# Performance work log

Hardware: AMD Instinct MI355X
Metric: run time of the kernel (lower is better)

## Reference

```python
import jax, jax.numpy as jnp
import numpy as np

B, D, H = 64, 768, 512            # batch, bert hidden, classifier hidden_dim
G0, C0 = 8192, 8                  # level-0 meta labels, children per meta
G1, C1 = 65536, 11                # level-1 meta labels, children per meta (incl. pad)
L = 670091                        # num labels; pad id == L, table has L+1 rows
K1, K2 = 32, 64                   # candidates_topk


def setup_inputs() -> dict:
    key = jax.random.key(0)
    ks = jax.random.split(key, 14)
    rn = lambda k, shp, s=1.0: jax.random.normal(k, shp, jnp.float32) * s
    w = 0.02  # xavier-ish init scale
    inp = {
        'feat5':   rn(ks[0], (B, D)),
        'feat8':   rn(ks[1], (B, D)),
        'featcat': rn(ks[2], (B, 3 * D)),
        'W0': rn(ks[3], (D, H), w),     'b0': jnp.zeros((H,), jnp.float32),
        'W1': rn(ks[4], (D, H), w),     'b1': jnp.zeros((H,), jnp.float32),
        'W2': rn(ks[5], (3 * D, H), w), 'b2': jnp.zeros((H,), jnp.float32),
        'E0': rn(ks[6], (G0, H), w),
        'E1': rn(ks[7], (G1, H), w),
        # padding row (index L) is zero, per self.Cn[-1].weight[-1].data.fill_(0)
        'E2': rn(ks[8], (L + 1, H), w).at[-1].set(0.0),
        'g0': jax.random.randint(ks[9], (G0, C0), 0, G1, dtype=jnp.int32),
        'g1': jax.random.randint(ks[10], (G1, C1), 0, L + 1, dtype=jnp.int32),
    }
    return inp


def reference(feat5, feat8, featcat, W0, b0, W1, b1, W2, b2, E0, E1, E2, g0, g1):
    gelu = lambda x: jax.nn.gelu(x, approximate=False)  # torch nn.GELU default (erf)
    # Cn_hidden (dropout is identity at eval)
    h0 = gelu(feat5 @ W0 + b0)      # [B,H]
    h1 = gelu(feat8 @ W1 + b1)      # [B,H]
    h2 = gelu(featcat @ W2 + b2)    # [B,H]

    # ---- level 0: score all G0 meta-labels (dense bmm) ----
    logits0 = jnp.einsum('gh,bh->bg', E0, h0)            # [B,G0]
    p0 = jax.nn.sigmoid(logits0)
    prev0 = jax.lax.stop_gradient(p0)                    # prev_logits = scores.detach()

    # ---- level 1: topk routing + gather + bmm ----
    sc1, idx1 = jax.lax.top_k(prev0, K1)                 # [B,K1]; prev_cands is arange -> identity map
    cands1 = g0[idx1].reshape(B, K1 * C0)                # [B,K1*C0] level-1 meta ids
    gsc1 = jnp.repeat(sc1, C0, axis=1)                   # candidates_scores flattened
    logits1 = jnp.einsum('bch,bh->bc', E1[cands1], h1)   # [B,K1*C0]
    p1 = jax.nn.sigmoid(logits1)
    w1 = p1 * gsc1
    prev1 = jax.lax.stop_gradient(p1)

    # ---- level 2 (final): topk routing into padded label groups ----
    sc2, idx2 = jax.lax.top_k(prev1, K2)                 # [B,K2]
    meta2 = jnp.take_along_axis(cands1, idx2, axis=1)    # indices into g1
    cands2 = g1[meta2].reshape(B, K2 * C1)               # [B,K2*C1] label ids (L == pad)
    gsc2 = jnp.repeat(sc2, C1, axis=1)
    logits2 = jnp.einsum('bch,bh->bc', E2[cands2], h2)   # pad rows of E2 are 0 -> logit 0
    # torch: where(logits==0, -inf, logits).sigmoid() -> pad positions score 0
    p2 = jnp.where(logits2 == 0.0, jnp.float32(0.0), jax.nn.sigmoid(logits2))
    w2 = p2 * gsc2

    return (p0, p1, p2, w1, w2, cands1, cands2)
```

## Files before the change

kernel.cpp:

```cpp
#include <hip/hip_runtime.h>
#include <math.h>

#define BB 64
#define D0 768
#define D2 2304
#define HH 512
#define BBHH (BB*HH)
#define NG0 8192
#define NC0 8
#define NCH1 11
#define TK1 32
#define TK2 64
#define NC1 (TK1*NC0)
#define NC2 (TK2*NCH1)
#define SP0 6
#define SP1 6
#define SP2 18

__device__ __forceinline__ float sigmoidf_(float x){ return 1.0f/(1.0f+expf(-x)); }
__device__ __forceinline__ float geluf_(float x){ return 0.5f*x*(1.0f+erff(x*0.70710678118654752f)); }
__device__ __forceinline__ unsigned long long maxu64_(unsigned long long a, unsigned long long b){ return a>b?a:b; }

__device__ __forceinline__ unsigned long long bitonic256_desc(
    unsigned long long key, int tid, unsigned long long* sbuf)
{
  #pragma unroll
  for (int k = 2; k <= 256; k <<= 1) {
    #pragma unroll
    for (int j = k >> 1; j > 0; j >>= 1) {
      unsigned long long other;
      if (j >= 64) {
        __syncthreads();
        sbuf[tid] = key;
        __syncthreads();
        other = sbuf[tid ^ j];
      } else {
        other = __shfl_xor(key, j, 64);
      }
      bool keep_max = ((tid & j) == 0) == ((tid & k) == 0);
      key = keep_max ? (key > other ? key : other)
                     : (key < other ? key : other);
    }
  }
  return key;
}

__global__ __launch_bounds__(256) void gemm_h_kernel(
    const float* __restrict__ feat5, const float* __restrict__ feat8,
    const float* __restrict__ featcat,
    const float* __restrict__ W0, const float* __restrict__ W1,
    const float* __restrict__ W2, float* __restrict__ P)
{
  int bid = blockIdx.x;
  const float* X; const float* W; int Dm, split, tile; float* Pb;
  if (bid < 48)      { X=feat5;   W=W0; Dm=D0; split=bid%6;  tile=bid/6;
                       Pb=P + (size_t)split*BBHH; }
  else if (bid < 96) { int l=bid-48; X=feat8; W=W1; Dm=D0; split=l%6; tile=l/6;
                       Pb=P + (size_t)(SP0+split)*BBHH; }
  else               { int l=bid-96; X=featcat; W=W2; Dm=D2; split=l%18; tile=l/18;
                       Pb=P + (size_t)(SP0+SP1+split)*BBHH; }
  int k0 = split*128;
  int jt = tile*64;
  __shared__ __align__(16) float At[32][68];
  __shared__ __align__(16) float Bt[32][68];
  int tid = threadIdx.x;
  int ti = tid >> 4, tj = tid & 15;
  float acc[4][4] = {};
  for (int ks = 0; ks < 128; ks += 32) {
    #pragma unroll
    for (int it = 0; it < 2; ++it) {
      int q = tid + it*256;
      int b = q & 63, kq = q >> 6;
      float4 v = *(const float4*)(X + (size_t)b*Dm + k0 + ks + kq*4);
      At[kq*4+0][b]=v.x; At[kq*4+1][b]=v.y; At[kq*4+2][b]=v.z; At[kq*4+3][b]=v.w;
    }
    #pragma unroll
    for (int it = 0; it < 2; ++it) {
      int q = tid + it*256;
      int j4 = q & 15, kk = q >> 4;
      float4 v = *(const float4*)(W + (size_t)(k0+ks+kk)*HH + jt + j4*4);
      *(float4*)&Bt[kk][j4*4] = v;
    }
    __syncthreads();
    #pragma unroll
    for (int k = 0; k < 32; ++k) {
      float4 a = *(const float4*)&At[k][ti*4];
      float4 b = *(const float4*)&Bt[k][tj*4];
      float av[4] = {a.x,a.y,a.z,a.w};
      float bv[4] = {b.x,b.y,b.z,b.w};
      #pragma unroll
      for (int r=0;r<4;++r)
        #pragma unroll
        for (int c=0;c<4;++c) acc[r][c] += av[r]*bv[c];
    }
    __syncthreads();
  }
  #pragma unroll
  for (int r=0;r<4;++r)
    #pragma unroll
    for (int c=0;c<4;++c) {
      int b = ti*4+r; int j = jt + tj*4 + c;
      Pb[(size_t)b*HH + j] = acc[r][c];
    }
}

__global__ __launch_bounds__(256) void level0_kernel(
    const float* __restrict__ P, const float* __restrict__ b0v,
    const float* __restrict__ E0, float* __restrict__ p0out)
{
  int bid = blockIdx.x;
  int btile = bid & 1;
  int gt = bid >> 1;
  __shared__ __align__(16) float At[32][36];
  __shared__ __align__(16) float Bt[32][68];
  int tid = threadIdx.x;
  int ti = tid >> 4, tj = tid & 15;
  float acc[2][4] = {};
  for (int ks = 0; ks < HH; ks += 32) {
    {
      int bb = tid & 31, kq = tid >> 5;
      float4 a = make_float4(0.f,0.f,0.f,0.f);
      #pragma unroll
      for (int s=0;s<SP0;++s){
        const float4 p = *(const float4*)(P + (size_t)s*BBHH
                           + (size_t)(btile*32+bb)*HH + ks + kq*4);
        a.x+=p.x; a.y+=p.y; a.z+=p.z; a.w+=p.w;
      }
      float4 bv = *(const float4*)(b0v + ks + kq*4);
      At[kq*4+0][bb]=geluf_(a.x+bv.x);
      At[kq*4+1][bb]=geluf_(a.y+bv.y);
      At[kq*4+2][bb]=geluf_(a.z+bv.z);
      At[kq*4+3][bb]=geluf_(a.w+bv.w);
    }
    #pragma unroll
    for (int it=0; it<2; ++it) {
      int q = tid + it*256; int g = q & 63, kq = q >> 6;
      float4 v = *(const float4*)(E0 + (size_t)(gt*64+g)*HH + ks + kq*4);
      Bt[kq*4+0][g]=v.x; Bt[kq*4+1][g]=v.y; Bt[kq*4+2][g]=v.z; Bt[kq*4+3][g]=v.w;
    }
    __syncthreads();
    #pragma unroll
    for (int k=0;k<32;++k) {
      float2 a = *(const float2*)&At[k][ti*2];
      float4 b = *(const float4*)&Bt[k][tj*4];
      float av[2] = {a.x,a.y};
      float bv[4] = {b.x,b.y,b.z,b.w};
      #pragma unroll
      for (int r=0;r<2;++r)
        #pragma unroll
        for (int c=0;c<4;++c) acc[r][c] += av[r]*bv[c];
    }
    __syncthreads();
  }
  #pragma unroll
  for (int r=0;r<2;++r)
    #pragma unroll
    for (int c=0;c<4;++c) {
      int b = btile*32 + ti*2 + r;
      int g = gt*64 + tj*4 + c;
      p0out[(size_t)b*NG0 + g] = sigmoidf_(acc[r][c]);
    }
}

__global__ __launch_bounds__(256) void topk1_kernel(
    const float* __restrict__ p0, const int* __restrict__ g0,
    const float* __restrict__ P, const float* __restrict__ b1v,
    float* __restrict__ h1out,
    int* __restrict__ cands1_i, float* __restrict__ gsc1, float* __restrict__ out_c1)
{
  int b = blockIdx.x, tid = threadIdx.x;
  {
    int j = tid*2;
    float ax=0.f, ay=0.f;
    #pragma unroll
    for (int s=0;s<SP1;++s){
      float2 v = *(const float2*)(P + (size_t)(SP0+s)*BBHH + (size_t)b*HH + j);
      ax += v.x; ay += v.y;
    }
    float2 bv = *(const float2*)(b1v + j);
    h1out[(size_t)b*HH + j]   = geluf_(ax + bv.x);
    h1out[(size_t)b*HH + j+1] = geluf_(ay + bv.y);
  }
  const float* row = p0 + (size_t)b*NG0;
  const float4* rp = (const float4*)(row + tid*32);
  unsigned long long m = 0ull;
  #pragma unroll
  for (int t=0;t<8;++t){
    float4 v = rp[t];
    unsigned i0 = (unsigned)(tid*32 + t*4);
    m = maxu64_(m, ((unsigned long long)__float_as_uint(v.x)<<32) | (unsigned long long)(0xFFFFFFFFu-(i0+0)));
    m = maxu64_(m, ((unsigned long long)__float_as_uint(v.y)<<32) | (unsigned long long)(0xFFFFFFFFu-(i0+1)));
    m = maxu64_(m, ((unsigned long long)__float_as_uint(v.z)<<32) | (unsigned long long)(0xFFFFFFFFu-(i0+2)));
    m = maxu64_(m, ((unsigned long long)__float_as_uint(v.w)<<32) | (unsigned long long)(0xFFFFFFFFu-(i0+3)));
  }
  __shared__ unsigned long long sbuf[256];
  __shared__ unsigned long long slist[256];
  __shared__ int scnt;
  __shared__ float s_sc[TK1];
  __shared__ int   s_idx[TK1];
  if (tid==0) scnt = 0;
  __syncthreads();
  unsigned long long sk = bitonic256_desc(m, tid, sbuf);
  __syncthreads();
  sbuf[tid] = sk;
  __syncthreads();
  unsigned long long t32 = sbuf[31];
  __syncthreads();
  #pragma unroll
  for (int t=0;t<8;++t){
    float4 v = rp[t];
    unsigned i0 = (unsigned)(tid*32 + t*4);
    unsigned long long k0 = ((unsigned long long)__float_as_uint(v.x)<<32) | (unsigned long long)(0xFFFFFFFFu-(i0+0));
    unsigned long long k1 = ((unsigned long long)__float_as_uint(v.y)<<32) | (unsigned long long)(0xFFFFFFFFu-(i0+1));
    unsigned long long k2 = ((unsigned long long)__float_as_uint(v.z)<<32) | (unsigned long long)(0xFFFFFFFFu-(i0+2));
    unsigned long long k3 = ((unsigned long long)__float_as_uint(v.w)<<32) | (unsigned long long)(0xFFFFFFFFu-(i0+3));
    if (k0 >= t32) { int p = atomicAdd(&scnt,1); if (p<256) slist[p]=k0; }
    if (k1 >= t32) { int p = atomicAdd(&scnt,1); if (p<256) slist[p]=k1; }
    if (k2 >= t32) { int p = atomicAdd(&scnt,1); if (p<256) slist[p]=k2; }
    if (k3 >= t32) { int p = atomicAdd(&scnt,1); if (p<256) slist[p]=k3; }
  }
  __syncthreads();
  int cnt = scnt;
  unsigned long long key2 = (tid < cnt) ? slist[tid] : 0ull;
  key2 = bitonic256_desc(key2, tid, sbuf);
  __syncthreads();
  sbuf[tid] = key2;
  __syncthreads();
  if (tid < TK1) {
    unsigned long long w = sbuf[tid];
    s_idx[tid] = (int)(0xFFFFFFFFu - (unsigned)(w & 0xFFFFFFFFull));
    s_sc[tid]  = __uint_as_float((unsigned)(w>>32));
  }
  __syncthreads();
  if (tid < NC1) {
    int k = tid >> 3, c = tid & 7;
    int cand = g0[(size_t)s_idx[k]*NC0 + c];
    cands1_i[(size_t)b*NC1+tid] = cand;
    gsc1[(size_t)b*NC1+tid] = s_sc[k];
    out_c1[(size_t)b*NC1+tid] = (float)cand;
  }
}

__global__ __launch_bounds__(256) void level1_kernel(
    const float* __restrict__ h1, const int* __restrict__ cands1_i,
    const float* __restrict__ gsc1, const float* __restrict__ E1,
    float* __restrict__ p1out, float* __restrict__ w1out)
{
  int b = blockIdx.x; int tid = threadIdx.x;
  int lane = tid & 63, wid = tid >> 6;
  const float4* h4 = (const float4*)(h1 + (size_t)b*HH);
  float4 ha = h4[lane*2], hb = h4[lane*2+1];
  int cbase = blockIdx.y*16 + wid*4;
  const int* ci = cands1_i + (size_t)b*NC1 + cbase;
  int id0=ci[0], id1=ci[1], id2=ci[2], id3=ci[3];
  const float4* e0 = (const float4*)(E1 + (size_t)id0*HH);
  const float4* e1 = (const float4*)(E1 + (size_t)id1*HH);
  const float4* e2 = (const float4*)(E1 + (size_t)id2*HH);
  const float4* e3 = (const float4*)(E1 + (size_t)id3*HH);
  float4 a0=e0[lane*2], c0=e0[lane*2+1];
  float4 a1=e1[lane*2], c1=e1[lane*2+1];
  float4 a2=e2[lane*2], c2=e2[lane*2+1];
  float4 a3=e3[lane*2], c3=e3[lane*2+1];
  float s0 = ha.x*a0.x+ha.y*a0.y+ha.z*a0.z+ha.w*a0.w + hb.x*c0.x+hb.y*c0.y+hb.z*c0.z+hb.w*c0.w;
  float s1 = ha.x*a1.x+ha.y*a1.y+ha.z*a1.z+ha.w*a1.w + hb.x*c1.x+hb.y*c1.y+hb.z*c1.z+hb.w*c1.w;
  float s2 = ha.x*a2.x+ha.y*a2.y+ha.z*a2.z+ha.w*a2.w + hb.x*c2.x+hb.y*c2.y+hb.z*c2.z+hb.w*c2.w;
  float s3 = ha.x*a3.x+ha.y*a3.y+ha.z*a3.z+ha.w*a3.w + hb.x*c3.x+hb.y*c3.y+hb.z*c3.z+hb.w*c3.w;
  #pragma unroll
  for (int off=1; off<64; off<<=1) {
    s0 += __shfl_xor(s0, off);
    s1 += __shfl_xor(s1, off);
    s2 += __shfl_xor(s2, off);
    s3 += __shfl_xor(s3, off);
  }
  if (lane==0) {
    const float* gs = gsc1 + (size_t)b*NC1 + cbase;
    float p;
    p = sigmoidf_(s0); p1out[(size_t)b*NC1+cbase+0]=p; w1out[(size_t)b*NC1+cbase+0]=p*gs[0];
    p = sigmoidf_(s1); p1out[(size_t)b*NC1+cbase+1]=p; w1out[(size_t)b*NC1+cbase+1]=p*gs[1];
    p = sigmoidf_(s2); p1out[(size_t)b*NC1+cbase+2]=p; w1out[(size_t)b*NC1+cbase+2]=p*gs[2];
    p = sigmoidf_(s3); p1out[(size_t)b*NC1+cbase+3]=p; w1out[(size_t)b*NC1+cbase+3]=p*gs[3];
  }
}

__global__ __launch_bounds__(256) void topk2_kernel(
    const float* __restrict__ p1, const int* __restrict__ cands1_i,
    const int* __restrict__ g1,
    const float* __restrict__ P, const float* __restrict__ b2v,
    float* __restrict__ h2out,
    int* __restrict__ cands2_i, float* __restrict__ gsc2, float* __restrict__ out_c2)
{
  int b = blockIdx.x, tid = threadIdx.x;
  {
    int j = tid*2;
    float ax=0.f, ay=0.f;
    #pragma unroll
    for (int s=0;s<SP2;++s){
      float2 v = *(const float2*)(P + (size_t)(SP0+SP1+s)*BBHH + (size_t)b*HH + j);
      ax += v.x; ay += v.y;
    }
    float2 bv = *(const float2*)(b2v + j);
    h2out[(size_t)b*HH + j]   = geluf_(ax + bv.x);
    h2out[(size_t)b*HH + j+1] = geluf_(ay + bv.y);
  }
  float v = p1[(size_t)b*NC1 + tid];
  unsigned long long key = ((unsigned long long)__float_as_uint(v)<<32) |
                           (unsigned long long)(0xFFFFFFFFu - (unsigned)tid);
  __shared__ unsigned long long sbuf[256];
  __shared__ float s_sc[TK2];
  __shared__ int   s_idx[TK2];
  key = bitonic256_desc(key, tid, sbuf);
  __syncthreads();
  sbuf[tid] = key;
  __syncthreads();
  if (tid < TK2) {
    unsigned long long w = sbuf[tid];
    s_idx[tid] = (int)(0xFFFFFFFFu - (unsigned)(w & 0xFFFFFFFFull));
    s_sc[tid]  = __uint_as_float((unsigned)(w>>32));
  }
  __syncthreads();
  for (int e=tid; e<NC2; e+=256) {
    int k = e/NCH1, c = e - k*NCH1;
    int meta = cands1_i[(size_t)b*NC1 + s_idx[k]];
    int cand = g1[(size_t)meta*NCH1 + c];
    cands2_i[(size_t)b*NC2+e] = cand;
    gsc2[(size_t)b*NC2+e] = s_sc[k];
    out_c2[(size_t)b*NC2+e] = (float)cand;
  }
}

__global__ __launch_bounds__(256) void level2_kernel(
    const float* __restrict__ h2, const int* __restrict__ cands2_i,
    const float* __restrict__ gsc2, const float* __restrict__ E2,
    float* __restrict__ p2out, float* __restrict__ w2out)
{
  int b = blockIdx.x; int tid = threadIdx.x;
  int lane = tid & 63, wid = tid >> 6;
  const float4* h4 = (const float4*)(h2 + (size_t)b*HH);
  float4 ha = h4[lane*2], hb = h4[lane*2+1];
  int cbase = blockIdx.y*16 + wid*4;
  const int* ci = cands2_i + (size_t)b*NC2 + cbase;
  int id0=ci[0], id1=ci[1], id2=ci[2], id3=ci[3];
  const float4* e0 = (const float4*)(E2 + (size_t)id0*HH);
  const float4* e1 = (const float4*)(E2 + (size_t)id1*HH);
  const float4* e2 = (const float4*)(E2 + (size_t)id2*HH);
  const float4* e3 = (const float4*)(E2 + (size_t)id3*HH);
  float4 a0=e0[lane*2], c0=e0[lane*2+1];
  float4 a1=e1[lane*2], c1=e1[lane*2+1];
  float4 a2=e2[lane*2], c2=e2[lane*2+1];
  float4 a3=e3[lane*2], c3=e3[lane*2+1];
  float s0 = ha.x*a0.x+ha.y*a0.y+ha.z*a0.z+ha.w*a0.w + hb.x*c0.x+hb.y*c0.y+hb.z*c0.z+hb.w*c0.w;
  float s1 = ha.x*a1.x+ha.y*a1.y+ha.z*a1.z+ha.w*a1.w + hb.x*c1.x+hb.y*c1.y+hb.z*c1.z+hb.w*c1.w;
  float s2 = ha.x*a2.x+ha.y*a2.y+ha.z*a2.z+ha.w*a2.w + hb.x*c2.x+hb.y*c2.y+hb.z*c2.z+hb.w*c2.w;
  float s3 = ha.x*a3.x+ha.y*a3.y+ha.z*a3.z+ha.w*a3.w + hb.x*c3.x+hb.y*c3.y+hb.z*c3.z+hb.w*c3.w;
  #pragma unroll
  for (int off=1; off<64; off<<=1) {
    s0 += __shfl_xor(s0, off);
    s1 += __shfl_xor(s1, off);
    s2 += __shfl_xor(s2, off);
    s3 += __shfl_xor(s3, off);
  }
  if (lane==0) {
    const float* gs = gsc2 + (size_t)b*NC2 + cbase;
    float p;
    p = (s0==0.0f)?0.0f:sigmoidf_(s0); p2out[(size_t)b*NC2+cbase+0]=p; w2out[(size_t)b*NC2+cbase+0]=p*gs[0];
    p = (s1==0.0f)?0.0f:sigmoidf_(s1); p2out[(size_t)b*NC2+cbase+1]=p; w2out[(size_t)b*NC2+cbase+1]=p*gs[1];
    p = (s2==0.0f)?0.0f:sigmoidf_(s2); p2out[(size_t)b*NC2+cbase+2]=p; w2out[(size_t)b*NC2+cbase+2]=p*gs[2];
    p = (s3==0.0f)?0.0f:sigmoidf_(s3); p2out[(size_t)b*NC2+cbase+3]=p; w2out[(size_t)b*NC2+cbase+3]=p*gs[3];
  }
}

extern "C" void kernel_launch(void* const* d_in, const int* in_sizes, int n_in,
                              void* d_out, int out_size, void* d_ws, size_t ws_size,
                              hipStream_t stream) {
  const float* feat5   = (const float*)d_in[0];
  const float* feat8   = (const float*)d_in[1];
  const float* featcat = (const float*)d_in[2];
  const float* W0 = (const float*)d_in[3];
  const float* b0 = (const float*)d_in[4];
  const float* W1 = (const float*)d_in[5];
  const float* b1 = (const float*)d_in[6];
  const float* W2 = (const float*)d_in[7];
  const float* b2 = (const float*)d_in[8];
  const float* E0 = (const float*)d_in[9];
  const float* E1 = (const float*)d_in[10];
  const float* E2 = (const float*)d_in[11];
  const int*   g0 = (const int*)d_in[12];
  const int*   g1 = (const int*)d_in[13];

  float* out = (float*)d_out;
  float* ws  = (float*)d_ws;

  size_t off = 0;
  float* P    = ws + off; off += (size_t)(SP0+SP1+SP2)*BBHH;
  float* hbuf = ws + off; off += 2ull*BBHH;
  int*   cands1_i = (int*)(ws + off); off += (size_t)BB*NC1;
  float* gsc1 = ws + off; off += (size_t)BB*NC1;
  int*   cands2_i = (int*)(ws + off); off += (size_t)BB*NC2;
  float* gsc2 = ws + off; off += (size_t)BB*NC2;

  float* h1 = hbuf;
  float* h2 = hbuf + BBHH;

  float* o_p0 = out;
  float* o_p1 = o_p0 + (size_t)BB*NG0;
  float* o_p2 = o_p1 + (size_t)BB*NC1;
  float* o_w1 = o_p2 + (size_t)BB*NC2;
  float* o_w2 = o_w1 + (size_t)BB*NC1;
  float* o_c1 = o_w2 + (size_t)BB*NC2;
  float* o_c2 = o_c1 + (size_t)BB*NC1;

  gemm_h_kernel<<<dim3(240), dim3(256), 0, stream>>>(feat5, feat8, featcat, W0, W1, W2, P);
  level0_kernel<<<dim3(256), dim3(256), 0, stream>>>(P, b0, E0, o_p0);
  topk1_kernel<<<dim3(64), dim3(256), 0, stream>>>(o_p0, g0, P, b1, h1, cands1_i, gsc1, o_c1);
  level1_kernel<<<dim3(64,16), dim3(256), 0, stream>>>(h1, cands1_i, gsc1, E1, o_p1, o_w1);
  topk2_kernel<<<dim3(64), dim3(256), 0, stream>>>(o_p1, cands1_i, g1, P, b2, h2, cands2_i, gsc2, o_c2);
  level2_kernel<<<dim3(64,44), dim3(256), 0, stream>>>(h2, cands2_i, gsc2, E2, o_p2, o_w2);
}
```

Measured before the change: 99.84 us.

## Fuse all six stages into one persistent kernel with software grid barriers

Replaces the six back-to-back kernel launches with a single persistent kernel of 256 blocks. The stages are separated by atomic-counter grid barriers in workspace, which is cleared with a memset before each launch. The aim is to remove per-launch overhead and inter-kernel gaps on a chain of small dependent stages. In exchange, the level-1 and level-2 gather work is folded onto fewer blocks with inner loops, only 64 blocks are active during the top-k phases, and the kernel relies on all 256 blocks being co-resident to avoid deadlock.

```diff
diff --git a/kernel.cpp b/kernel.cpp
--- a/kernel.cpp
+++ b/kernel.cpp
@@ -16,10 +16,29 @@
 #define SP0 6
 #define SP1 6
 #define SP2 18
+#define NBLK 256
 
 __device__ __forceinline__ float sigmoidf_(float x){ return 1.0f/(1.0f+expf(-x)); }
 __device__ __forceinline__ float geluf_(float x){ return 0.5f*x*(1.0f+erff(x*0.70710678118654752f)); }
 __device__ __forceinline__ unsigned long long maxu64_(unsigned long long a, unsigned long long b){ return a>b?a:b; }
+
+__device__ __forceinline__ void gridbar(unsigned* bar, int slot){
+  __syncthreads();
+  if (threadIdx.x==0){
+    unsigned* cnt  = bar + (size_t)slot*32;
+    unsigned* flag = cnt + 16;
+    __threadfence();
+    unsigned old = __hip_atomic_fetch_add(cnt, 1u, __ATOMIC_ACQ_REL, __HIP_MEMORY_SCOPE_AGENT);
+    if (old == NBLK-1u){
+      __hip_atomic_store(flag, 1u, __ATOMIC_RELEASE, __HIP_MEMORY_SCOPE_AGENT);
+    } else {
+      while (__hip_atomic_load(flag, __ATOMIC_ACQUIRE, __HIP_MEMORY_SCOPE_AGENT) == 0u)
+        __builtin_amdgcn_s_sleep(8);
+    }
+    __threadfence();
+  }
+  __syncthreads();
+}
 
 __device__ __forceinline__ unsigned long long bitonic256_desc(
     unsigned long long key, int tid, unsigned long long* sbuf)
@@ -45,327 +64,331 @@
   return key;
 }
 
-__global__ __launch_bounds__(256) void gemm_h_kernel(
+__global__ __launch_bounds__(256) void mega_kernel(
     const float* __restrict__ feat5, const float* __restrict__ feat8,
     const float* __restrict__ featcat,
-    const float* __restrict__ W0, const float* __restrict__ W1,
-    const float* __restrict__ W2, float* __restrict__ P)
+    const float* __restrict__ W0, const float* __restrict__ b0v,
+    const float* __restrict__ W1, const float* __restrict__ b1v,
+    const float* __restrict__ W2, const float* __restrict__ b2v,
+    const float* __restrict__ E0, const float* __restrict__ E1,
+    const float* __restrict__ E2,
+    const int* __restrict__ g0, const int* __restrict__ g1,
+    unsigned* __restrict__ bar,
+    float* __restrict__ P, float* __restrict__ h1buf, float* __restrict__ h2buf,
+    int* __restrict__ cands1_i, float* __restrict__ gsc1,
+    int* __restrict__ cands2_i, float* __restrict__ gsc2,
+    float* __restrict__ o_p0, float* __restrict__ o_p1, float* __restrict__ o_p2,
+    float* __restrict__ o_w1, float* __restrict__ o_w2,
+    float* __restrict__ o_c1, float* __restrict__ o_c2)
 {
-  int bid = blockIdx.x;
-  const float* X; const float* W; int Dm, split, tile; float* Pb;
-  if (bid < 48)      { X=feat5;   W=W0; Dm=D0; split=bid%6;  tile=bid/6;
-                       Pb=P + (size_t)split*BBHH; }
-  else if (bid < 96) { int l=bid-48; X=feat8; W=W1; Dm=D0; split=l%6; tile=l/6;
-                       Pb=P + (size_t)(SP0+split)*BBHH; }
-  else               { int l=bid-96; X=featcat; W=W2; Dm=D2; split=l%18; tile=l/18;
-                       Pb=P + (size_t)(SP0+SP1+split)*BBHH; }
-  int k0 = split*128;
-  int jt = tile*64;
-  __shared__ __align__(16) float At[32][68];
-  __shared__ __align__(16) float Bt[32][68];
-  int tid = threadIdx.x;
-  int ti = tid >> 4, tj = tid & 15;
-  float acc[4][4] = {};
-  for (int ks = 0; ks < 128; ks += 32) {
-    #pragma unroll
-    for (int it = 0; it < 2; ++it) {
-      int q = tid + it*256;
-      int b = q & 63, kq = q >> 6;
-      float4 v = *(const float4*)(X + (size_t)b*Dm + k0 + ks + kq*4);
-      At[kq*4+0][b]=v.x; At[kq*4+1][b]=v.y; At[kq*4+2][b]=v.z; At[kq*4+3][b]=v.w;
-    }
-    #pragma unroll
-    for (int it = 0; it < 2; ++it) {
-      int q = tid + it*256;
-      int j4 = q & 15, kk = q >> 4;
-      float4 v = *(const float4*)(W + (size_t)(k0+ks+kk)*HH + jt + j4*4);
-      *(float4*)&Bt[kk][j4*4] = v;
-    }
-    __syncthreads();
-    #pragma unroll
-    for (int k = 0; k < 32; ++k) {
-      float4 a = *(const float4*)&At[k][ti*4];
-      float4 b = *(const float4*)&Bt[k][tj*4];
-      float av[4] = {a.x,a.y,a.z,a.w};
-      float bv[4] = {b.x,b.y,b.z,b.w};
-      #pragma unroll
-      for (int r=0;r<4;++r)
+  __shared__ __align__(16) char smem[17408];
+  const int bid = blockIdx.x;
+  const int tid = threadIdx.x;
+  const int lane = tid & 63, wid = tid >> 6;
+
+  if (bid < 240) {
+    const float* X; const float* W; int Dm, split, tile; float* Pb;
+    if (bid < 48)      { X=feat5;   W=W0; Dm=D0; split=bid%6;  tile=bid/6;
+                         Pb=P + (size_t)split*BBHH; }
+    else if (bid < 96) { int l=bid-48; X=feat8; W=W1; Dm=D0; split=l%6; tile=l/6;
+                         Pb=P + (size_t)(SP0+split)*BBHH; }
+    else               { int l=bid-96; X=featcat; W=W2; Dm=D2; split=l%18; tile=l/18;
+                         Pb=P + (size_t)(SP0+SP1+split)*BBHH; }
+    int k0 = split*128;
+    int jt = tile*64;
+    float (*At)[68] = (float(*)[68])smem;
+    float (*Bt)[68] = (float(*)[68])(smem + 8704);
+    int ti = tid >> 4, tj = tid & 15;
+    float acc[4][4] = {};
+    for (int ks = 0; ks < 128; ks += 32) {
+      #pragma unroll
+      for (int it = 0; it < 2; ++it) {
+        int q = tid + it*256;
+        int b = q & 63, kq = q >> 6;
+        float4 v = *(const float4*)(X + (size_t)b*Dm + k0 + ks + kq*4);
+        At[kq*4+0][b]=v.x; At[kq*4+1][b]=v.y; At[kq*4+2][b]=v.z; At[kq*4+3][b]=v.w;
+      }
+      #pragma unroll
+      for (int it = 0; it < 2; ++it) {
+        int q = tid + it*256;
+        int j4 = q & 15, kk = q >> 4;
+        float4 v = *(const float4*)(W + (size_t)(k0+ks+kk)*HH + jt + j4*4);
+        *(float4*)&Bt[kk][j4*4] = v;
+      }
+      __syncthreads();
+      #pragma unroll
+      for (int k = 0; k < 32; ++k) {
+        float4 a = *(const float4*)&At[k][ti*4];
+        float4 b = *(const float4*)&Bt[k][tj*4];
+        float av[4] = {a.x,a.y,a.z,a.w};
+        float bv[4] = {b.x,b.y,b.z,b.w};
         #pragma unroll
-        for (int c=0;c<4;++c) acc[r][c] += av[r]*bv[c];
-    }
-    __syncthreads();
-  }
-  #pragma unroll
-  for (int r=0;r<4;++r)
-    #pragma unroll
-    for (int c=0;c<4;++c) {
-      int b = ti*4+r; int j = jt + tj*4 + c;
-      Pb[(size_t)b*HH + j] = acc[r][c];
-    }
-}
-
-__global__ __launch_bounds__(256) void level0_kernel(
-    const float* __restrict__ P, const float* __restrict__ b0v,
-    const float* __restrict__ E0, float* __restrict__ p0out)
-{
-  int bid = blockIdx.x;
-  int btile = bid & 1;
-  int gt = bid >> 1;
-  __shared__ __align__(16) float At[32][36];
-  __shared__ __align__(16) float Bt[32][68];
-  int tid = threadIdx.x;
-  int ti = tid >> 4, tj = tid & 15;
-  float acc[2][4] = {};
-  for (int ks = 0; ks < HH; ks += 32) {
+        for (int r=0;r<4;++r)
+          #pragma unroll
+          for (int c=0;c<4;++c) acc[r][c] += av[r]*bv[c];
+      }
+      __syncthreads();
+    }
+    #pragma unroll
+    for (int r=0;r<4;++r)
+      #pragma unroll
+      for (int c=0;c<4;++c)
+        Pb[(size_t)(ti*4+r)*HH + jt + tj*4 + c] = acc[r][c];
+  }
+
+  gridbar(bar, 0);
+
+  {
+    int btile = bid & 1;
+    int gt = bid >> 1;
+    float (*At)[36] = (float(*)[36])smem;
+    float (*Bt)[68] = (float(*)[68])(smem + 4608);
+    int ti = tid >> 4, tj = tid & 15;
+    float acc[2][4] = {};
+    for (int ks = 0; ks < HH; ks += 32) {
+      {
+        int bb = tid & 31, kq = tid >> 5;
+        float4 a = make_float4(0.f,0.f,0.f,0.f);
+        #pragma unroll
+        for (int s=0;s<SP0;++s){
+          const float4 p = *(const float4*)(P + (size_t)s*BBHH
+                             + (size_t)(btile*32+bb)*HH + ks + kq*4);
+          a.x+=p.x; a.y+=p.y; a.z+=p.z; a.w+=p.w;
+        }
+        float4 bv = *(const float4*)(b0v + ks + kq*4);
+        At[kq*4+0][bb]=geluf_(a.x+bv.x);
+        At[kq*4+1][bb]=geluf_(a.y+bv.y);
+        At[kq*4+2][bb]=geluf_(a.z+bv.z);
+        At[kq*4+3][bb]=geluf_(a.w+bv.w);
+      }
+      #pragma unroll
+      for (int it=0; it<2; ++it) {
+        int q = tid + it*256; int g = q & 63, kq = q >> 6;
+        float4 v = *(const float4*)(E0 + (size_t)(gt*64+g)*HH + ks + kq*4);
+        Bt[kq*4+0][g]=v.x; Bt[kq*4+1][g]=v.y; Bt[kq*4+2][g]=v.z; Bt[kq*4+3][g]=v.w;
+      }
+      __syncthreads();
+      #pragma unroll
+      for (int k=0;k<32;++k) {
+        float2 a = *(const float2*)&At[k][ti*2];
+        float4 b = *(const float4*)&Bt[k][tj*4];
+        float av[2] = {a.x,a.y};
+        float bv[4] = {b.x,b.y,b.z,b.w};
+        #pragma unroll
+        for (int r=0;r<2;++r)
+          #pragma unroll
+          for (int c=0;c<4;++c) acc[r][c] += av[r]*bv[c];
+      }
+      __syncthreads();
+    }
+    #pragma unroll
+    for (int r=0;r<2;++r)
+      #pragma unroll
+      for (int c=0;c<4;++c)
+        o_p0[(size_t)(btile*32 + ti*2 + r)*NG0 + gt*64 + tj*4 + c] = sigmoidf_(acc[r][c]);
+  }
+
+  gridbar(bar, 1);
+
+  if (bid < 64) {
+    int b = bid;
     {
-      int bb = tid & 31, kq = tid >> 5;
-      float4 a = make_float4(0.f,0.f,0.f,0.f);
-      #pragma unroll
-      for (int s=0;s<SP0;++s){
-        const float4 p = *(const float4*)(P + (size_t)s*BBHH
-                           + (size_t)(btile*32+bb)*HH + ks + kq*4);
-        a.x+=p.x; a.y+=p.y; a.z+=p.z; a.w+=p.w;
-      }
-      float4 bv = *(const float4*)(b0v + ks + kq*4);
-      At[kq*4+0][bb]=geluf_(a.x+bv.x);
-      At[kq*4+1][bb]=geluf_(a.y+bv.y);
-      At[kq*4+2][bb]=geluf_(a.z+bv.z);
-      At[kq*4+3][bb]=geluf_(a.w+bv.w);
-    }
-    #pragma unroll
-    for (int it=0; it<2; ++it) {
-      int q = tid + it*256; int g = q & 63, kq = q >> 6;
-      float4 v = *(const float4*)(E0 + (size_t)(gt*64+g)*HH + ks + kq*4);
-      Bt[kq*4+0][g]=v.x; Bt[kq*4+1][g]=v.y; Bt[kq*4+2][g]=v.z; Bt[kq*4+3][g]=v.w;
-    }
-    __syncthreads();
-    #pragma unroll
-    for (int k=0;k<32;++k) {
-      float2 a = *(const float2*)&At[k][ti*2];
-      float4 b = *(const float4*)&Bt[k][tj*4];
-      float av[2] = {a.x,a.y};
-      float bv[4] = {b.x,b.y,b.z,b.w};
-      #pragma unroll
-      for (int r=0;r<2;++r)
-        #pragma unroll
-        for (int c=0;c<4;++c) acc[r][c] += av[r]*bv[c];
-    }
-    __syncthreads();
-  }
-  #pragma unroll
-  for (int r=0;r<2;++r)
-    #pragma unroll
-    for (int c=0;c<4;++c) {
-      int b = btile*32 + ti*2 + r;
-      int g = gt*64 + tj*4 + c;
-      p0out[(size_t)b*NG0 + g] = sigmoidf_(acc[r][c]);
-    }
-}
-
-__global__ __launch_bounds__(256) void topk1_kernel(
-    const float* __restrict__ p0, const int* __restrict__ g0,
-    const float* __restrict__ P, const float* __restrict__ b1v,
-    float* __restrict__ h1out,
-    int* __restrict__ cands1_i, float* __restrict__ gsc1, float* __restrict__ out_c1)
-{
-  int b = blockIdx.x, tid = threadIdx.x;
+      int j = tid*2;
+      float ax=0.f, ay=0.f;
+      #pragma unroll
+      for (int s=0;s<SP1;++s){
+        float2 v = *(const float2*)(P + (size_t)(SP0+s)*BBHH + (size_t)b*HH + j);
+        ax += v.x; ay += v.y;
+      }
+      float2 bv = *(const float2*)(b1v + j);
+      h1buf[(size_t)b*HH + j]   = geluf_(ax + bv.x);
+      h1buf[(size_t)b*HH + j+1] = geluf_(ay + bv.y);
+    }
+    const float* row = o_p0 + (size_t)b*NG0;
+    const float4* rp = (const float4*)(row + tid*32);
+    unsigned long long m = 0ull;
+    #pragma unroll
+    for (int t=0;t<8;++t){
+      float4 v = rp[t];
+      unsigned i0 = (unsigned)(tid*32 + t*4);
+      m = maxu64_(m, ((unsigned long long)__float_as_uint(v.x)<<32) | (unsigned long long)(0xFFFFFFFFu-(i0+0)));
+      m = maxu64_(m, ((unsigned long long)__float_as_uint(v.y)<<32) | (unsigned long long)(0xFFFFFFFFu-(i0+1)));
+      m = maxu64_(m, ((unsigned long long)__float_as_uint(v.z)<<32) | (unsigned long long)(0xFFFFFFFFu-(i0+2)));
+      m = maxu64_(m, ((unsigned long long)__float_as_uint(v.w)<<32) | (unsigned long long)(0xFFFFFFFFu-(i0+3)));
+    }
+    unsigned long long* sbuf  = (unsigned long long*)smem;
+    unsigned long long* slist = (unsigned long long*)(smem + 2048);
+    float* s_sc = (float*)(smem + 4096);
+    int*   s_idx = (int*)(smem + 4224);
+    int*   scnt = (int*)(smem + 4352);
+    if (tid==0) *scnt = 0;
+    __syncthreads();
+    unsigned long long sk = bitonic256_desc(m, tid, sbuf);
+    __syncthreads();
+    sbuf[tid] = sk;
+    __syncthreads();
+    unsigned long long t32 = sbuf[31];
+    __syncthreads();
+    #pragma unroll
+    for (int t=0;t<8;++t){
+      float4 v = rp[t];
+      unsigned i0 = (unsigned)(tid*32 + t*4);
+      unsigned long long k0 = ((unsigned long long)__float_as_uint(v.x)<<32) | (unsigned long long)(0xFFFFFFFFu-(i0+0));
+      unsigned long long k1 = ((unsigned long long)__float_as_uint(v.y)<<32) | (unsigned long long)(0xFFFFFFFFu-(i0+1));
+      unsigned long long k2 = ((unsigned long long)__float_as_uint(v.z)<<32) | (unsigned long long)(0xFFFFFFFFu-(i0+2));
+      unsigned long long k3 = ((unsigned long long)__float_as_uint(v.w)<<32) | (unsigned long long)(0xFFFFFFFFu-(i0+3));
+      if (k0 >= t32) { int p = atomicAdd(scnt,1); if (p<256) slist[p]=k0; }
+      if (k1 >= t32) { int p = atomicAdd(scnt,1); if (p<256) slist[p]=k1; }
+      if (k2 >= t32) { int p = atomicAdd(scnt,1); if (p<256) slist[p]=k2; }
+      if (k3 >= t32) { int p = atomicAdd(scnt,1); if (p<256) slist[p]=k3; }
+    }
+    __syncthreads();
+    int cnt = *scnt;
+    unsigned long long key2 = (tid < cnt) ? slist[tid] : 0ull;
+    key2 = bitonic256_desc(key2, tid, sbuf);
+    __syncthreads();
+    sbuf[tid] = key2;
+    __syncthreads();
+    if (tid < TK1) {
+      unsigned long long w = sbuf[tid];
+      s_idx[tid] = (int)(0xFFFFFFFFu - (unsigned)(w & 0xFFFFFFFFull));
+      s_sc[tid]  = __uint_as_float((unsigned)(w>>32));
+    }
+    __syncthreads();
+    if (tid < NC1) {
+      int k = tid >> 3, c = tid & 7;
+      int cand = g0[(size_t)s_idx[k]*NC0 + c];
+      cands1_i[(size_t)b*NC1+tid] = cand;
+      gsc1[(size_t)b*NC1+tid] = s_sc[k];
+      out_of_line: ;
+      o_c1[(size_t)b*NC1+tid] = (float)cand;
+    }
+  }
+
+  gridbar(bar, 2);
+
   {
-    int j = tid*2;
-    float ax=0.f, ay=0.f;
-    #pragma unroll
-    for (int s=0;s<SP1;++s){
-      float2 v = *(const float2*)(P + (size_t)(SP0+s)*BBHH + (size_t)b*HH + j);
-      ax += v.x; ay += v.y;
-    }
-    float2 bv = *(const float2*)(b1v + j);
-    h1out[(size_t)b*HH + j]   = geluf_(ax + bv.x);
-    h1out[(size_t)b*HH + j+1] = geluf_(ay + bv.y);
-  }
-  const float* row = p0 + (size_t)b*NG0;
-  const float4* rp = (const float4*)(row + tid*32);
-  unsigned long long m = 0ull;
-  #pragma unroll
-  for (int t=0;t<8;++t){
-    float4 v = rp[t];
-    unsigned i0 = (unsigned)(tid*32 + t*4);
-    m = maxu64_(m, ((unsigned long long)__float_as_uint(v.x)<<32) | (unsigned long long)(0xFFFFFFFFu-(i0+0)));
-    m = maxu64_(m, ((unsigned long long)__float_as_uint(v.y)<<32) | (unsigned long long)(0xFFFFFFFFu-(i0+1)));
-    m = maxu64_(m, ((unsigned long long)__float_as_uint(v.z)<<32) | (unsigned long long)(0xFFFFFFFFu-(i0+2)));
-    m = maxu64_(m, ((unsigned long long)__float_as_uint(v.w)<<32) | (unsigned long long)(0xFFFFFFFFu-(i0+3)));
-  }
-  __shared__ unsigned long long sbuf[256];
-  __shared__ unsigned long long slist[256];
-  __shared__ int scnt;
-  __shared__ float s_sc[TK1];
-  __shared__ int   s_idx[TK1];
-  if (tid==0) scnt = 0;
-  __syncthreads();
-  unsigned long long sk = bitonic256_desc(m, tid, sbuf);
-  __syncthreads();
-  sbuf[tid] = sk;
-  __syncthreads();
-  unsigned long long t32 = sbuf[31];
-  __syncthreads();
-  #pragma unroll
-  for (int t=0;t<8;++t){
-    float4 v = rp[t];
-    unsigned i0 = (unsigned)(tid*32 + t*4);
-    unsigned long long k0 = ((unsigned long long)__float_as_uint(v.x)<<32) | (unsigned long long)(0xFFFFFFFFu-(i0+0));
-    unsigned long long k1 = ((unsigned long long)__float_as_uint(v.y)<<32) | (unsigned long long)(0xFFFFFFFFu-(i0+1));
-    unsigned long long k2 = ((unsigned long long)__float_as_uint(v.z)<<32) | (unsigned long long)(0xFFFFFFFFu-(i0+2));
-    unsigned long long k3 = ((unsigned long long)__float_as_uint(v.w)<<32) | (unsigned long long)(0xFFFFFFFFu-(i0+3));
-    if (k0 >= t32) { int p = atomicAdd(&scnt,1); if (p<256) slist[p]=k0; }
-    if (k1 >= t32) { int p = atomicAdd(&scnt,1); if (p<256) slist[p]=k1; }
-    if (k2 >= t32) { int p = atomicAdd(&scnt,1); if (p<256) slist[p]=k2; }
-    if (k3 >= t32) { int p = atomicAdd(&scnt,1); if (p<256) slist[p]=k3; }
-  }
-  __syncthreads();
-  int cnt = scnt;
-  unsigned long long key2 = (tid < cnt) ? slist[tid] : 0ull;
-  key2 = bitonic256_desc(key2, tid, sbuf);
-  __syncthreads();
-  sbuf[tid] = key2;
-  __syncthreads();
-  if (tid < TK1) {
-    unsigned long long w = sbuf[tid];
-    s_idx[tid] = (int)(0xFFFFFFFFu - (unsigned)(w & 0xFFFFFFFFull));
-    s_sc[tid]  = __uint_as_float((unsigned)(w>>32));
-  }
-  __syncthreads();
-  if (tid < NC1) {
-    int k = tid >> 3, c = tid & 7;
-    int cand = g0[(size_t)s_idx[k]*NC0 + c];
-    cands1_i[(size_t)b*NC1+tid] = cand;
-    gsc1[(size_t)b*NC1+tid] = s_sc[k];
-    out_c1[(size_t)b*NC1+tid] = (float)cand;
-  }
-}
-
-__global__ __launch_bounds__(256) void level1_kernel(
-    const float* __restrict__ h1, const int* __restrict__ cands1_i,
-    const float* __restrict__ gsc1, const float* __restrict__ E1,
-    float* __restrict__ p1out, float* __restrict__ w1out)
-{
-  int b = blockIdx.x; int tid = threadIdx.x;
-  int lane = tid & 63, wid = tid >> 6;
-  const float4* h4 = (const float4*)(h1 + (size_t)b*HH);
-  float4 ha = h4[lane*2], hb = h4[lane*2+1];
-  int cbase = blockIdx.y*16 + wid*4;
-  const int* ci = cands1_i + (size_t)b*NC1 + cbase;
-  int id0=ci[0], id1=ci[1], id2=ci[2], id3=ci[3];
-  const float4* e0 = (const float4*)(E1 + (size_t)id0*HH);
-  const float4* e1 = (const float4*)(E1 + (size_t)id1*HH);
-  const float4* e2 = (const float4*)(E1 + (size_t)id2*HH);
-  const float4* e3 = (const float4*)(E1 + (size_t)id3*HH);
-  float4 a0=e0[lane*2], c0=e0[lane*2+1];
-  float4 a1=e1[lane*2], c1=e1[lane*2+1];
-  float4 a2=e2[lane*2], c2=e2[lane*2+1];
-  float4 a3=e3[lane*2], c3=e3[lane*2+1];
-  float s0 = ha.x*a0.x+ha.y*a0.y+ha.z*a0.z+ha.w*a0.w + hb.x*c0.x+hb.y*c0.y+hb.z*c0.z+hb.w*c0.w;
-  float s1 = ha.x*a1.x+ha.y*a1.y+ha.z*a1.z+ha.w*a1.w + hb.x*c1.x+hb.y*c1.y+hb.z*c1.z+hb.w*c1.w;
-  float s2 = ha.x*a2.x+ha.y*a2.y+ha.z*a2.z+ha.w*a2.w + hb.x*c2.x+hb.y*c2.y+hb.z*c2.z+hb.w*c2.w;
-  float s3 = ha.x*a3.x+ha.y*a3.y+ha.z*a3.z+ha.w*a3.w + hb.x*c3.x+hb.y*c3.y+hb.z*c3.z+hb.w*c3.w;
-  #pragma unroll
-  for (int off=1; off<64; off<<=1) {
-    s0 += __shfl_xor(s0, off);
-    s1 += __shfl_xor(s1, off);
-    s2 += __shfl_xor(s2, off);
-    s3 += __shfl_xor(s3, off);
-  }
-  if (lane==0) {
-    const float* gs = gsc1 + (size_t)b*NC1 + cbase;
-    float p;
-    p = sigmoidf_(s0); p1out[(size_t)b*NC1+cbase+0]=p; w1out[(size_t)b*NC1+cbase+0]=p*gs[0];
-    p = sigmoidf_(s1); p1out[(size_t)b*NC1+cbase+1]=p; w1out[(size_t)b*NC1+cbase+1]=p*gs[1];
-    p = sigmoidf_(s2); p1out[(size_t)b*NC1+cbase+2]=p; w1out[(size_t)b*NC1+cbase+2]=p*gs[2];
-    p = sigmoidf_(s3); p1out[(size_t)b*NC1+cbase+3]=p; w1out[(size_t)b*NC1+cbase+3]=p*gs[3];
-  }
-}
-
-__global__ __launch_bounds__(256) void topk2_kernel(
-    const float* __restrict__ p1, const int* __restrict__ cands1_i,
-    const int* __restrict__ g1,
-    const float* __restrict__ P, const float* __restrict__ b2v,
-    float* __restrict__ h2out,
-    int* __restrict__ cands2_i, float* __restrict__ gsc2, float* __restrict__ out_c2)
-{
-  int b = blockIdx.x, tid = threadIdx.x;
+    int b = bid & 63;
+    const float4* h4 = (const float4*)(h1buf + (size_t)b*HH);
+    float4 ha = h4[lane*2], hb = h4[lane*2+1];
+    #pragma unroll
+    for (int j=0;j<4;++j){
+      int ytile = (bid >> 6) + 4*j;
+      int cbase = ytile*16 + wid*4;
+      const int* ci = cands1_i + (size_t)b*NC1 + cbase;
+      int id0=ci[0], id1=ci[1], id2=ci[2], id3=ci[3];
+      const float4* e0 = (const float4*)(E1 + (size_t)id0*HH);
+      const float4* e1 = (const float4*)(E1 + (size_t)id1*HH);
+      const float4* e2 = (const float4*)(E1 + (size_t)id2*HH);
+      const float4* e3 = (const float4*)(E1 + (size_t)id3*HH);
+      float4 a0=e0[lane*2], c0=e0[lane*2+1];
+      float4 a1=e1[lane*2], c1=e1[lane*2+1];
+      float4 a2=e2[lane*2], c2=e2[lane*2+1];
+      float4 a3=e3[lane*2], c3=e3[lane*2+1];
+      float s0 = ha.x*a0.x+ha.y*a0.y+ha.z*a0.z+ha.w*a0.w + hb.x*c0.x+hb.y*c0.y+hb.z*c0.z+hb.w*c0.w;
+      float s1 = ha.x*a1.x+ha.y*a1.y+ha.z*a1.z+ha.w*a1.w + hb.x*c1.x+hb.y*c1.y+hb.z*c1.z+hb.w*c1.w;
+      float s2 = ha.x*a2.x+ha.y*a2.y+ha.z*a2.z+ha.w*a2.w + hb.x*c2.x+hb.y*c2.y+hb.z*c2.z+hb.w*c2.w;
+      float s3 = ha.x*a3.x+ha.y*a3.y+ha.z*a3.z+ha.w*a3.w + hb.x*c3.x+hb.y*c3.y+hb.z*c3.z+hb.w*c3.w;
+      #pragma unroll
+      for (int off=1; off<64; off<<=1) {
+        s0 += __shfl_xor(s0, off);
+        s1 += __shfl_xor(s1, off);
+        s2 += __shfl_xor(s2, off);
+        s3 += __shfl_xor(s3, off);
+      }
+      if (lane==0) {
+        const float* gs = gsc1 + (size_t)b*NC1 + cbase;
+        float p;
+        p = sigmoidf_(s0); o_p1[(size_t)b*NC1+cbase+0]=p; o_w1[(size_t)b*NC1+cbase+0]=p*gs[0];
+        p = sigmoidf_(s1); o_p1[(size_t)b*NC1+cbase+1]=p; o_w1[(size_t)b*NC1+cbase+1]=p*gs[1];
+        p = sigmoidf_(s2); o_p1[(size_t)b*NC1+cbase+2]=p; o_w1[(size_t)b*NC1+cbase+2]=p*gs[2];
+        p = sigmoidf_(s3); o_p1[(size_t)b*NC1+cbase+3]=p; o_w1[(size_t)b*NC1+cbase+3]=p*gs[3];
+      }
+    }
+  }
+
+  gridbar(bar, 3);
+
+  if (bid < 64) {
+    int b = bid;
+    {
+      int j = tid*2;
+      float ax=0.f, ay=0.f;
+      #pragma unroll
+      for (int s=0;s<SP2;++s){
+        float2 v = *(const float2*)(P + (size_t)(SP0+SP1+s)*BBHH + (size_t)b*HH + j);
+        ax += v.x; ay += v.y;
+      }
+      float2 bv = *(const float2*)(b2v + j);
+      h2buf[(size_t)b*HH + j]   = geluf_(ax + bv.x);
+      h2buf[(size_t)b*HH + j+1] = geluf_(ay + bv.y);
+    }
+    float v = o_p1[(size_t)b*NC1 + tid];
+    unsigned long long key = ((unsigned long long)__float_as_uint(v)<<32) |
+                             (unsigned long long)(0xFFFFFFFFu - (unsigned)tid);
+    unsigned long long* sbuf = (unsigned long long*)smem;
+    float* s_sc = (float*)(smem + 2048);
+    int*   s_idx = (int*)(smem + 2304);
+    key = bitonic256_desc(key, tid, sbuf);
+    __syncthreads();
+    sbuf[tid] = key;
+    __syncthreads();
+    if (tid < TK2) {
+      unsigned long long w = sbuf[tid];
+      s_idx[tid] = (int)(0xFFFFFFFFu - (unsigned)(w & 0xFFFFFFFFull));
+      s_sc[tid]  = __uint_as_float((unsigned)(w>>32));
+    }
+    __syncthreads();
+    for (int e=tid; e<NC2; e+=256) {
+      int k = e/NCH1, c = e - k*NCH1;
+      int meta = cands1_i[(size_t)b*NC1 + s_idx[k]];
+      int cand = g1[(size_t)meta*NCH1 + c];
+      cands2_i[(size_t)b*NC2+e] = cand;
+      gsc2[(size_t)b*NC2+e] = s_sc[k];
+      o_c2[(size_t)b*NC2+e] = (float)cand;
+    }
+  }
+
+  gridbar(bar, 4);
+
   {
-    int j = tid*2;
-    float ax=0.f, ay=0.f;
-    #pragma unroll
-    for (int s=0;s<SP2;++s){
-      float2 v = *(const float2*)(P + (size_t)(SP0+SP1+s)*BBHH + (size_t)b*HH + j);
-      ax += v.x; ay += v.y;
-    }
-    float2 bv = *(const float2*)(b2v + j);
-    h2out[(size_t)b*HH + j]   = geluf_(ax + bv.x);
-    h2out[(size_t)b*HH + j+1] = geluf_(ay + bv.y);
-  }
-  float v = p1[(size_t)b*NC1 + tid];
-  unsigned long long key = ((unsigned long long)__float_as_uint(v)<<32) |
-                           (unsigned long long)(0xFFFFFFFFu - (unsigned)tid);
-  __shared__ unsigned long long sbuf[256];
-  __shared__ float s_sc[TK2];
-  __shared__ int   s_idx[TK2];
-  key = bitonic256_desc(key, tid, sbuf);
-  __syncthreads();
-  sbuf[tid] = key;
-  __syncthreads();
-  if (tid < TK2) {
-    unsigned long long w = sbuf[tid];
-    s_idx[tid] = (int)(0xFFFFFFFFu - (unsigned)(w & 0xFFFFFFFFull));
-    s_sc[tid]  = __uint_as_float((unsigned)(w>>32));
-  }
-  __syncthreads();
-  for (int e=tid; e<NC2; e+=256) {
-    int k = e/NCH1, c = e - k*NCH1;
-    int meta = cands1_i[(size_t)b*NC1 + s_idx[k]];
-    int cand = g1[(size_t)meta*NCH1 + c];
-    cands2_i[(size_t)b*NC2+e] = cand;
-    gsc2[(size_t)b*NC2+e] = s_sc[k];
-    out_c2[(size_t)b*NC2+e] = (float)cand;
-  }
-}
-
-__global__ __launch_bounds__(256) void level2_kernel(
-    const float* __restrict__ h2, const int* __restrict__ cands2_i,
-    const float* __restrict__ gsc2, const float* __restrict__ E2,
-    float* __restrict__ p2out, float* __restrict__ w2out)
-{
-  int b = blockIdx.x; int tid = threadIdx.x;
-  int lane = tid & 63, wid = tid >> 6;
-  const float4* h4 = (const float4*)(h2 + (size_t)b*HH);
-  float4 ha = h4[lane*2], hb = h4[lane*2+1];
-  int cbase = blockIdx.y*16 + wid*4;
-  const int* ci = cands2_i + (size_t)b*NC2 + cbase;
-  int id0=ci[0], id1=ci[1], id2=ci[2], id3=ci[3];
-  const float4* e0 = (const float4*)(E2 + (size_t)id0*HH);
-  const float4* e1 = (const float4*)(E2 + (size_t)id1*HH);
-  const float4* e2 = (const float4*)(E2 + (size_t)id2*HH);
-  const float4* e3 = (const float4*)(E2 + (size_t)id3*HH);
-  float4 a0=e0[lane*2], c0=e0[lane*2+1];
-  float4 a1=e1[lane*2], c1=e1[lane*2+1];
-  float4 a2=e2[lane*2], c2=e2[lane*2+1];
-  float4 a3=e3[lane*2], c3=e3[lane*2+1];
-  float s0 = ha.x*a0.x+ha.y*a0.y+ha.z*a0.z+ha.w*a0.w + hb.x*c0.x+hb.y*c0.y+hb.z*c0.z+hb.w*c0.w;
-  float s1 = ha.x*a1.x+ha.y*a1.y+ha.z*a1.z+ha.w*a1.w + hb.x*c1.x+hb.y*c1.y+hb.z*c1.z+hb.w*c1.w;
-  float s2 = ha.x*a2.x+ha.y*a2.y+ha.z*a2.z+ha.w*a2.w + hb.x*c2.x+hb.y*c2.y+hb.z*c2.z+hb.w*c2.w;
-  float s3 = ha.x*a3.x+ha.y*a3.y+ha.z*a3.z+ha.w*a3.w + hb.x*c3.x+hb.y*c3.y+hb.z*c3.z+hb.w*c3.w;
-  #pragma unroll
-  for (int off=1; off<64; off<<=1) {
-    s0 += __shfl_xor(s0, off);
-    s1 += __shfl_xor(s1, off);
-    s2 += __shfl_xor(s2, off);
-    s3 += __shfl_xor(s3, off);
-  }
-  if (lane==0) {
-    const float* gs = gsc2 + (size_t)b*NC2 + cbase;
-    float p;
-    p = (s0==0.0f)?0.0f:sigmoidf_(s0); p2out[(size_t)b*NC2+cbase+0]=p; w2out[(size_t)b*NC2+cbase+0]=p*gs[0];
-    p = (s1==0.0f)?0.0f:sigmoidf_(s1); p2out[(size_t)b*NC2+cbase+1]=p; w2out[(size_t)b*NC2+cbase+1]=p*gs[1];
-    p = (s2==0.0f)?0.0f:sigmoidf_(s2); p2out[(size_t)b*NC2+cbase+2]=p; w2out[(size_t)b*NC2+cbase+2]=p*gs[2];
-    p = (s3==0.0f)?0.0f:sigmoidf_(s3); p2out[(size_t)b*NC2+cbase+3]=p; w2out[(size_t)b*NC2+cbase+3]=p*gs[3];
+    int b = bid & 63;
+    const float4* h4 = (const float4*)(h2buf + (size_t)b*HH);
+    float4 ha = h4[lane*2], hb = h4[lane*2+1];
+    #pragma unroll
+    for (int j=0;j<11;++j){
+      int ytile = (bid >> 6) + 4*j;
+      int cbase = ytile*16 + wid*4;
+      const int* ci = cands2_i + (size_t)b*NC2 + cbase;
+      int id0=ci[0], id1=ci[1], id2=ci[2], id3=ci[3];
+      const float4* e0 = (const float4*)(E2 + (size_t)id0*HH);
+      const float4* e1 = (const float4*)(E2 + (size_t)id1*HH);
+      const float4* e2 = (const float4*)(E2 + (size_t)id2*HH);
+      const float4* e3 = (const float4*)(E2 + (size_t)id3*HH);
+      float4 a0=e0[lane*2], c0=e0[lane*2+1];
+      float4 a1=e1[lane*2], c1=e1[lane*2+1];
+      float4 a2=e2[lane*2], c2=e2[lane*2+1];
+      float4 a3=e3[lane*2], c3=e3[lane*2+1];
+      float s0 = ha.x*a0.x+ha.y*a0.y+ha.z*a0.z+ha.w*a0.w + hb.x*c0.x+hb.y*c0.y+hb.z*c0.z+hb.w*c0.w;
+      float s1 = ha.x*a1.x+ha.y*a1.y+ha.z*a1.z+ha.w*a1.w + hb.x*c1.x+hb.y*c1.y+hb.z*c1.z+hb.w*c1.w;
+      float s2 = ha.x*a2.x+ha.y*a2.y+ha.z*a2.z+ha.w*a2.w + hb.x*c2.x+hb.y*c2.y+hb.z*c2.z+hb.w*c2.w;
+      float s3 = ha.x*a3.x+ha.y*a3.y+ha.z*a3.z+ha.w*a3.w + hb.x*c3.x+hb.y*c3.y+hb.z*c3.z+hb.w*c3.w;
+      #pragma unroll
+      for (int off=1; off<64; off<<=1) {
+        s0 += __shfl_xor(s0, off);
+        s1 += __shfl_xor(s1, off);
+        s2 += __shfl_xor(s2, off);
+        s3 += __shfl_xor(s3, off);
+      }
+      if (lane==0) {
+        const float* gs = gsc2 + (size_t)b*NC2 + cbase;
+        float p;
+        p = (s0==0.0f)?0.0f:sigmoidf_(s0); o_p2[(size_t)b*NC2+cbase+0]=p; o_w2[(size_t)b*NC2+cbase+0]=p*gs[0];
+        p = (s1==0.0f)?0.0f:sigmoidf_(s1); o_p2[(size_t)b*NC2+cbase+1]=p; o_w2[(size_t)b*NC2+cbase+1]=p*gs[1];
+        p = (s2==0.0f)?0.0f:sigmoidf_(s2); o_p2[(size_t)b*NC2+cbase+2]=p; o_w2[(size_t)b*NC2+cbase+2]=p*gs[2];
+        p = (s3==0.0f)?0.0f:sigmoidf_(s3); o_p2[(size_t)b*NC2+cbase+3]=p; o_w2[(size_t)b*NC2+cbase+3]=p*gs[3];
+      }
+    }
   }
 }
 
@@ -391,15 +414,14 @@
   float* ws  = (float*)d_ws;
 
   size_t off = 0;
+  unsigned* bar = (unsigned*)(ws);        off += 256;
   float* P    = ws + off; off += (size_t)(SP0+SP1+SP2)*BBHH;
-  float* hbuf = ws + off; off += 2ull*BBHH;
+  float* h1   = ws + off; off += BBHH;
+  float* h2   = ws + off; off += BBHH;
   int*   cands1_i = (int*)(ws + off); off += (size_t)BB*NC1;
   float* gsc1 = ws + off; off += (size_t)BB*NC1;
   int*   cands2_i = (int*)(ws + off); off += (size_t)BB*NC2;
   float* gsc2 = ws + off; off += (size_t)BB*NC2;
-
-  float* h1 = hbuf;
-  float* h2 = hbuf + BBHH;
 
   float* o_p0 = out;
   float* o_p1 = o_p0 + (size_t)BB*NG0;
@@ -409,10 +431,9 @@
   float* o_c1 = o_w2 + (size_t)BB*NC2;
   float* o_c2 = o_c1 + (size_t)BB*NC1;
 
-  gemm_h_kernel<<<dim3(240), dim3(256), 0, stream>>>(feat5, feat8, featcat, W0, W1, W2, P);
-  level0_kernel<<<dim3(256), dim3(256), 0, stream>>>(P, b0, E0, o_p0);
-  topk1_kernel<<<dim3(64), dim3(256), 0, stream>>>(o_p0, g0, P, b1, h1, cands1_i, gsc1, o_c1);
-  level1_kernel<<<dim3(64,16), dim3(256), 0, stream>>>(h1, cands1_i, gsc1, E1, o_p1, o_w1);
-  topk2_kernel<<<dim3(64), dim3(256), 0, stream>>>(o_p1, cands1_i, g1, P, b2, h2, cands2_i, gsc2, o_c2);
-  level2_kernel<<<dim3(64,44), dim3(256), 0, stream>>>(h2, cands2_i, gsc2, E2, o_p2, o_w2);
+  hipMemsetAsync(bar, 0, 1024, stream);
+  mega_kernel<<<dim3(NBLK), dim3(256), 0, stream>>>(
+      feat5, feat8, featcat, W0, b0, W1, b1, W2, b2, E0, E1, E2, g0, g1,
+      bar, P, h1, h2, cands1_i, gsc1, cands2_i, gsc2,
+      o_p0, o_p1, o_p2, o_w1, o_w2, o_c1, o_c2);
 }
```

After: 266.0 us. 2.66x slower.
